# Kernel tuning notes

Hardware: AMD Instinct MI355X
Metric: run time of the kernel (lower is better)

The kernel has to match this reference:

```python
import jax, jax.numpy as jnp
import numpy as np

T, B, I, H, C, O = 4096, 8, 256, 512, 1024, 512
SCHEDULE = 1.0
UPPER_T = 0.3
NIND = int((1.0 - SCHEDULE) * (C - 2) * UPPER_T) + 1  # = 1 (argmax WTA)


def setup_inputs() -> dict:
    key = jax.random.key(0)
    ks = jax.random.split(key, 8)
    def lin(k, fan_out, fan_in):
        s = 1.0 / np.sqrt(fan_in)
        kw, kb = jax.random.split(k)
        return (jax.random.uniform(kw, (fan_out, fan_in), jnp.float32, -s, s),
                jax.random.uniform(kb, (fan_out,), jnp.float32, -s, s))
    i2m_w, i2m_b = lin(ks[0], H, I)
    m2h_w, m2h_b = lin(ks[1], C, H)
    h2o_w, h2o_b = lin(ks[2], O, C)
    return {
        "x": jax.random.normal(ks[3], (T, B, I), jnp.float32),
        "hidden1": jnp.zeros((1,), jnp.float32),  # unused dummy (overwritten in torch forward)
        "i2m_w": i2m_w, "i2m_b": i2m_b,
        "m2h_w": m2h_w, "m2h_b": m2h_b,
        "h2o_w": h2o_w, "h2o_b": h2o_b,
    }


def reference(x, hidden1, i2m_w, i2m_b, m2h_w, m2h_b, h2o_w, h2o_b):
    # linear -> relu
    h = jax.nn.relu(jnp.einsum('tbi,hi->tbh', x, i2m_w) + i2m_b)
    # linear -> relu -> concept pre-activations [T,B,C]
    c = jax.nn.relu(jnp.einsum('tbh,ch->tbc', h, m2h_w) + m2h_b)
    # winner-take-all: top-Nind scatter mask (replaces CPU argsort round-trip)
    _, idx = jax.lax.top_k(c, NIND)  # [T,B,NIND]
    t_ix = jnp.arange(c.shape[0])[:, None, None]
    b_ix = jnp.arange(c.shape[1])[None, :, None]
    mask = jnp.zeros_like(c).at[t_ix, b_ix, idx].set(1.0)
    m = c * mask
    # L2 normalize over concept axis
    m = m / jnp.linalg.norm(m, axis=-1, keepdims=True)
    out = jnp.einsum('tbc,oc->tbo', m, h2o_w) + h2o_b
    return jax.nn.log_softmax(out, axis=-1)
```

## Files before the change

### kernel.cpp

```cpp
#include <hip/hip_runtime.h>
#include <stdint.h>

#define M_ROWS 32768
#define I_DIM 256
#define H_DIM 512
#define C_DIM 1024
#define O_DIM 512

typedef __attribute__((ext_vector_type(8))) short bf16x8;
typedef __attribute__((ext_vector_type(4))) float f32x4;

__device__ __forceinline__ ushort bf16_rne(float f) {
    unsigned u = __float_as_uint(f);
    unsigned r = u + 0x7FFFu + ((u >> 16) & 1u);
    return (ushort)(r >> 16);
}
__device__ __forceinline__ float bf16_f32(ushort h) {
    return __uint_as_float(((unsigned)h) << 16);
}
__device__ __forceinline__ void split2(float f, ushort& hi, ushort& mid) {
    hi = bf16_rne(f);
    mid = bf16_rne(f - bf16_f32(hi));
}

__device__ __forceinline__ void async_ld16(const void* g, void* l) {
    __builtin_amdgcn_global_load_lds(
        (const __attribute__((address_space(1))) void*)g,
        (__attribute__((address_space(3))) void*)l, 16, 0, 0);
}

__device__ __forceinline__ unsigned long long packvi(float v, int col) {
    unsigned u = __float_as_uint(v);
    u = (u & 0x80000000u) ? ~u : (u | 0x80000000u);
    return ((unsigned long long)u << 32) | (unsigned)(~col);
}

__device__ __forceinline__ int slot_of(int kc, int row) {
    return (kc + ((row >> 1) & 3)) & 3;
}

__global__ __launch_bounds__(256)
void prep(const float* __restrict__ W1, ushort* __restrict__ w1h, ushort* __restrict__ w1m,
          const float* __restrict__ W2, ushort* __restrict__ w2h, ushort* __restrict__ w2m,
          const float* __restrict__ Wo, const float* __restrict__ bo,
          float* __restrict__ LS, unsigned long long* __restrict__ part) {
    __shared__ float sred[4];
    const int b = blockIdx.x;
    const int t = threadIdx.x;
    if (b < 320) {
        const int isW1 = (b < 64);
        const float* W = isW1 ? W1 : W2;
        ushort* hh = isW1 ? w1h : w2h;
        ushort* mm = isW1 ? w1m : w2m;
        const int K = isW1 ? I_DIM : H_DIM;
        const int cpr = K >> 3;
        int gid = (isW1 ? b : b - 64) * 256 + t;
        int row = gid / cpr;
        int rem = gid - row * cpr;
        int g = rem >> 2, kc = rem & 3;
        float4 v0 = *(const float4*)(W + (size_t)gid * 8);
        float4 v1 = *(const float4*)(W + (size_t)gid * 8 + 4);
        __align__(16) ushort h[8], m[8];
        float f[8];
        *(float4*)&f[0] = v0; *(float4*)&f[4] = v1;
        #pragma unroll
        for (int j = 0; j < 8; ++j) split2(f[j], h[j], m[j]);
        size_t dst = (size_t)row * K + g * 32 + slot_of(kc, row) * 8;
        *(uint4*)(hh + dst) = *(uint4*)h;
        *(uint4*)(mm + dst) = *(uint4*)m;
    } else if (b < 1344) {
        const int j = b - 320;
        float l0 = Wo[(size_t)t * C_DIM + j] + bo[t];
        float l1 = Wo[(size_t)(t + 256) * C_DIM + j] + bo[t + 256];

        float mx = fmaxf(l0, l1);
        #pragma unroll
        for (int off = 1; off < 64; off <<= 1)
            mx = fmaxf(mx, __shfl_xor(mx, off, 64));
        if ((t & 63) == 0) sred[t >> 6] = mx;
        __syncthreads();
        mx = fmaxf(fmaxf(sred[0], sred[1]), fmaxf(sred[2], sred[3]));
        __syncthreads();

        float s = expf(l0 - mx) + expf(l1 - mx);
        #pragma unroll
        for (int off = 1; off < 64; off <<= 1)
            s += __shfl_xor(s, off, 64);
        if ((t & 63) == 0) sred[t >> 6] = s;
        __syncthreads();
        s = sred[0] + sred[1] + sred[2] + sred[3];

        float lse = mx + logf(s);
        LS[(size_t)j * O_DIM + t] = l0 - lse;
        LS[(size_t)j * O_DIM + t + 256] = l1 - lse;
    } else {
        part[(b - 1344) * 256 + t] = 0ull;
    }
}

__global__ __launch_bounds__(256, 4)
void gemm1_mfma(const float* __restrict__ X, const ushort* __restrict__ W1h,
                const ushort* __restrict__ W1m, const float* __restrict__ b1,
                ushort* __restrict__ Hh, ushort* __restrict__ Hm) {
    __shared__ __align__(16) ushort LB[16384];
    ushort* As0 = LB;
    ushort* As1 = LB + 4096;
    ushort* Bs0 = LB + 8192;
    ushort* Bs1 = LB + 12288;

    const int tid = threadIdx.x;
    const int lane = tid & 63, wave = tid >> 6;
    const int wm = wave >> 1, wn = wave & 1;
    const int lcol = lane & 15, quad = lane >> 4;
    const int mBase = blockIdx.x * 128;
    const int nBase = blockIdx.y * 128;
    const int s_row = tid >> 1, s_half = tid & 1;
    const int bplane = wave >> 1;
    const ushort* wp = bplane ? W1m : W1h;
    const int brow0 = (wave & 1) * 64;
    const int lrow = lane >> 2, lk = (lane & 3) * 8;

    f32x4 acc[4][4];
    #pragma unroll
    for (int i = 0; i < 4; ++i)
        #pragma unroll
        for (int j = 0; j < 4; ++j)
            acc[i][j] = (f32x4){0.f, 0.f, 0.f, 0.f};

    int aoff[4], boff[4];
    #pragma unroll
    for (int t = 0; t < 4; ++t) {
        int ra = wm * 64 + t * 16 + lcol;
        int rb = wn * 64 + t * 16 + lcol;
        aoff[t] = ra * 32 + slot_of(quad, ra) * 8;
        boff[t] = rb * 32 + slot_of(quad, rb) * 8;
    }
    const int sl0 = slot_of(s_half * 2,     s_row);
    const int sl1 = slot_of(s_half * 2 + 1, s_row);

    for (int ks = 0; ks < I_DIM / 32; ++ks) {
        const int k0 = ks * 32;
        const float* ap = X + (size_t)(mBase + s_row) * I_DIM + k0 + s_half * 16;
        float4 f0 = ((const float4*)ap)[0];
        float4 f1 = ((const float4*)ap)[1];
        float4 f2 = ((const float4*)ap)[2];
        float4 f3 = ((const float4*)ap)[3];

        __syncthreads();

        #pragma unroll
        for (int i = 0; i < 4; ++i) {
            int r = brow0 + i * 16;
            const ushort* g = wp + (size_t)(nBase + r + lrow) * I_DIM + k0 + lk;
            async_ld16(g, (bplane ? Bs1 : Bs0) + r * 32);
        }

        float f[16];
        *(float4*)&f[0] = f0; *(float4*)&f[4] = f1;
        *(float4*)&f[8] = f2; *(float4*)&f[12] = f3;
        bf16x8 h0, h1, m0, m1;
        #pragma unroll
        for (int j = 0; j < 8; ++j) {
            ushort hu, mu;
            split2(f[j], hu, mu);
            h0[j] = (short)hu; m0[j] = (short)mu;
            split2(f[j + 8], hu, mu);
            h1[j] = (short)hu; m1[j] = (short)mu;
        }
        *(bf16x8*)&As0[s_row * 32 + sl0 * 8] = h0;
        *(bf16x8*)&As0[s_row * 32 + sl1 * 8] = h1;
        *(bf16x8*)&As1[s_row * 32 + sl0 * 8] = m0;
        *(bf16x8*)&As1[s_row * 32 + sl1 * 8] = m1;

        __syncthreads();

        bf16x8 af[4][2];
        #pragma unroll
        for (int mt = 0; mt < 4; ++mt) {
            af[mt][0] = *(const bf16x8*)&As0[aoff[mt]];
            af[mt][1] = *(const bf16x8*)&As1[aoff[mt]];
        }
        #pragma unroll
        for (int nt = 0; nt < 4; ++nt) {
            bf16x8 bh = *(const bf16x8*)&Bs0[boff[nt]];
            bf16x8 bm = *(const bf16x8*)&Bs1[boff[nt]];
            #pragma unroll
            for (int mt = 0; mt < 4; ++mt) {
                f32x4 a = acc[mt][nt];
                a = __builtin_amdgcn_mfma_f32_16x16x32_bf16(af[mt][1], bh, a, 0, 0, 0);
                a = __builtin_amdgcn_mfma_f32_16x16x32_bf16(af[mt][0], bm, a, 0, 0, 0);
                a = __builtin_amdgcn_mfma_f32_16x16x32_bf16(af[mt][0], bh, a, 0, 0, 0);
                acc[mt][nt] = a;
            }
        }
    }

    #pragma unroll
    for (int plane = 0; plane < 2; ++plane) {
        __syncthreads();
        #pragma unroll
        for (int nt = 0; nt < 4; ++nt) {
            int colRel = wn * 64 + nt * 16 + lcol;
            int g = colRel >> 5, kc = (colRel >> 3) & 3, pos = colRel & 7;
            float bias = b1[nBase + colRel];
            #pragma unroll
            for (int mt = 0; mt < 4; ++mt) {
                #pragma unroll
                for (int r = 0; r < 4; ++r) {
                    int rowRel = wm * 64 + mt * 16 + quad * 4 + r;
                    float v = fmaxf(acc[mt][nt][r] + bias, 0.f);
                    ushort hu, mu;
                    split2(v, hu, mu);
                    LB[rowRel * 128 + g * 32 + slot_of(kc, rowRel) * 8 + pos]
                        = plane ? mu : hu;
                }
            }
        }
        __syncthreads();
        ushort* dstp = plane ? Hm : Hh;
        #pragma unroll
        for (int l = 0; l < 8; ++l) {
            int c = l * 256 + tid;
            int row = c >> 4, idx = c & 15;
            *(uint4*)(dstp + (size_t)(mBase + row) * H_DIM + nBase + idx * 8)
                = *(const uint4*)&LB[row * 128 + idx * 8];
        }
    }
}

__global__ __launch_bounds__(512, 2)
void gemm2_mfma(const ushort* __restrict__ Hh, const ushort* __restrict__ Hm,
                const ushort* __restrict__ W2h, const ushort* __restrict__ W2m,
                const float* __restrict__ b2,
                unsigned long long* __restrict__ part) {
    __shared__ __align__(16) ushort As[2][2][8192];
    __shared__ __align__(16) ushort Bs[2][2][8192];
    const int tid = threadIdx.x;
    const int lane = tid & 63, wave = tid >> 6;
    const int wm = wave >> 2, wn = wave & 3;
    const int lcol = lane & 15, quad = lane >> 4;
    const int lrow = lane >> 2, lk = (lane & 3) * 8;

    const int d = blockIdx.x;
    const int l = d >> 3;
    const int mT = ((d & 7) << 4) + (l >> 2);
    const int nT = l & 3;
    const int mBase = mT * 256;
    const int nBase = nT * 256;

    const int m_id = wave >> 1;
    const int shalf = wave & 1;
    const ushort* gsrc;
    ushort* l0;
    ushort* l1;
    switch (m_id) {
        case 0:  gsrc = Hh  + (size_t)mBase * H_DIM; l0 = &As[0][0][0]; l1 = &As[1][0][0]; break;
        case 1:  gsrc = Hm  + (size_t)mBase * H_DIM; l0 = &As[0][1][0]; l1 = &As[1][1][0]; break;
        case 2:  gsrc = W2h + (size_t)nBase * H_DIM; l0 = &Bs[0][0][0]; l1 = &Bs[1][0][0]; break;
        default: gsrc = W2m + (size_t)nBase * H_DIM; l0 = &Bs[0][1][0]; l1 = &Bs[1][1][0]; break;
    }
    l0 += shalf * 4096;
    l1 += shalf * 4096;
    const ushort* gks = gsrc + (size_t)(shalf * 128 + lrow) * H_DIM + lk;

    f32x4 acc[8][4];
    #pragma unroll
    for (int i = 0; i < 8; ++i)
        #pragma unroll
        for (int j = 0; j < 4; ++j)
            acc[i][j] = (f32x4){0.f, 0.f, 0.f, 0.f};

    int aoff[8], boff[4];
    #pragma unroll
    for (int t = 0; t < 8; ++t) {
        int ra = wm * 128 + t * 16 + lcol;
        aoff[t] = ra * 32 + slot_of(quad, ra) * 8;
    }
    #pragma unroll
    for (int t = 0; t < 4; ++t) {
        int rb = wn * 64 + t * 16 + lcol;
        boff[t] = rb * 32 + slot_of(quad, rb) * 8;
    }

    auto stage = [&](ushort* lb, int k0) {
        #pragma unroll
        for (int j = 0; j < 8; ++j)
            async_ld16(gks + k0 + (size_t)(j * 16) * H_DIM, lb + j * 512);
    };

    stage(l0, 0);
    asm volatile("s_waitcnt vmcnt(0)" ::: "memory");
    __builtin_amdgcn_s_barrier();
    __builtin_amdgcn_sched_barrier(0);

    const int NK = H_DIM / 32;
    #pragma unroll 2
    for (int ks = 0; ks < NK; ++ks) {
        const int cur = ks & 1;
        if (ks < NK - 1) {
            stage(cur ? l0 : l1, (ks + 1) * 32);
            __builtin_amdgcn_sched_barrier(0);
        }

        bf16x8 bh[4], bm[4];
        #pragma unroll
        for (int nt = 0; nt < 4; ++nt) {
            bh[nt] = *(const bf16x8*)&Bs[cur][0][boff[nt]];
            bm[nt] = *(const bf16x8*)&Bs[cur][1][boff[nt]];
        }
        #pragma unroll
        for (int half = 0; half < 2; ++half) {
            bf16x8 ah[4], am[4];
            #pragma unroll
            for (int mt = 0; mt < 4; ++mt) {
                ah[mt] = *(const bf16x8*)&As[cur][0][aoff[half * 4 + mt]];
                am[mt] = *(const bf16x8*)&As[cur][1][aoff[half * 4 + mt]];
            }
            __builtin_amdgcn_s_setprio(1);
            #pragma unroll
            for (int nt = 0; nt < 4; ++nt) {
                #pragma unroll
                for (int mt = 0; mt < 4; ++mt) {
                    f32x4 a = acc[half * 4 + mt][nt];
                    a = __builtin_amdgcn_mfma_f32_16x16x32_bf16(am[mt], bh[nt], a, 0, 0, 0);
                    a = __builtin_amdgcn_mfma_f32_16x16x32_bf16(ah[mt], bm[nt], a, 0, 0, 0);
                    a = __builtin_amdgcn_mfma_f32_16x16x32_bf16(ah[mt], bh[nt], a, 0, 0, 0);
                    acc[half * 4 + mt][nt] = a;
                }
            }
            __builtin_amdgcn_s_setprio(0);
        }

        if (ks < NK - 1)
            asm volatile("s_waitcnt vmcnt(0)" ::: "memory");
        __builtin_amdgcn_s_barrier();
        __builtin_amdgcn_sched_barrier(0);
    }

    float bias[4];
    #pragma unroll
    for (int nt = 0; nt < 4; ++nt)
        bias[nt] = b2[nBase + wn * 64 + nt * 16 + lcol];

    #pragma unroll
    for (int mt = 0; mt < 8; ++mt) {
        #pragma unroll
        for (int r = 0; r < 4; ++r) {
            unsigned long long best = 0ull;
            #pragma unroll
            for (int nt = 0; nt < 4; ++nt) {
                int col = nBase + wn * 64 + nt * 16 + lcol;
                float v = acc[mt][nt][r] + bias[nt];
                unsigned long long p = packvi(v, col);
                if (p > best) best = p;
            }
            #pragma unroll
            for (int off = 1; off < 16; off <<= 1) {
                unsigned long long o = __shfl_xor((long long)best, off, 64);
                if (o > best) best = o;
            }
            if (lcol == 0) {
                int row = mBase + wm * 128 + mt * 16 + quad * 4 + r;
                atomicMax(&part[row], best);
            }
        }
    }
}

__global__ __launch_bounds__(256)
void gather_out(const unsigned long long* __restrict__ part,
                const float* __restrict__ LS, float* __restrict__ out) {
    const int tid = threadIdx.x;
    const int row = blockIdx.x * 2 + (tid >> 7);
    const int q = tid & 127;
    unsigned long long best = part[row];
    unsigned u = (unsigned)(best >> 32);
    float v = (u & 0x80000000u) ? __uint_as_float(u ^ 0x80000000u)
                                : __uint_as_float(~u);
    int col = (int)(~(unsigned)best) & (C_DIM - 1);
    int j = (v > 0.f) ? col : 0;
    float4 val = ((const float4*)LS)[(size_t)j * 128 + q];
    ((float4*)out)[(size_t)row * 128 + q] = val;
}

extern "C" void kernel_launch(void* const* d_in, const int* in_sizes, int n_in,
                              void* d_out, int out_size, void* d_ws, size_t ws_size,
                              hipStream_t stream) {
    const float* x     = (const float*)d_in[0];
    const float* i2m_w = (const float*)d_in[2];
    const float* i2m_b = (const float*)d_in[3];
    const float* m2h_w = (const float*)d_in[4];
    const float* m2h_b = (const float*)d_in[5];
    const float* h2o_w = (const float*)d_in[6];
    const float* h2o_b = (const float*)d_in[7];
    float* out = (float*)d_out;

    char* ws = (char*)d_ws;
    ushort* w1h = (ushort*)(ws);
    ushort* w1m = (ushort*)(ws + 262144);
    ushort* w2h = (ushort*)(ws + 524288);
    ushort* w2m = (ushort*)(ws + 1572864);
    float*  LS  = (float*)(ws + 2621440);
    unsigned long long* part = (unsigned long long*)(ws + 4718592);

    ushort* Hh = (ushort*)d_out;
    ushort* Hm = Hh + (size_t)M_ROWS * H_DIM;

    prep<<<1472, 256, 0, stream>>>(i2m_w, w1h, w1m, m2h_w, w2h, w2m,
                                   h2o_w, h2o_b, LS, part);
    gemm1_mfma<<<dim3(M_ROWS / 128, H_DIM / 128), 256, 0, stream>>>(
        x, w1h, w1m, i2m_b, Hh, Hm);
    gemm2_mfma<<<(M_ROWS / 256) * (C_DIM / 256), 512, 0, stream>>>(
        Hh, Hm, w2h, w2m, m2h_b, part);
    gather_out<<<M_ROWS / 2, 256, 0, stream>>>(part, LS, out);
}
```

Measured before the change: 244.5 us.

## Split GEMM k-step into four phases interleaving LDS reads, async loads and MFMAs

Restructures the inner k-loop of the concept GEMM into four sub-phases, each covering a quarter of the output tile. Each phase issues its own LDS fragment reads. The next tile's global-to-LDS async loads are split across the first two phases, with barriers placed so the waves stay in lockstep. The aim is to spread memory traffic evenly between MFMA bursts and to lower register pressure by holding fewer B fragments at once. In exchange it adds more barriers per k-step and reloads the A fragments twice.

```diff
diff --git a/kernel.cpp b/kernel.cpp
--- a/kernel.cpp
+++ b/kernel.cpp
@@ -282,13 +282,15 @@
         boff[t] = rb * 32 + slot_of(quad, rb) * 8;
     }
 
-    auto stage = [&](ushort* lb, int k0) {
-        #pragma unroll
-        for (int j = 0; j < 8; ++j)
-            async_ld16(gks + k0 + (size_t)(j * 16) * H_DIM, lb + j * 512);
+    auto stage4 = [&](ushort* lb, int k0, int jb) {
+        #pragma unroll
+        for (int j = 0; j < 4; ++j)
+            async_ld16(gks + k0 + (size_t)((jb + j) * 16) * H_DIM,
+                       lb + (jb + j) * 512);
     };
 
-    stage(l0, 0);
+    stage4(l0, 0, 0);
+    stage4(l0, 0, 4);
     asm volatile("s_waitcnt vmcnt(0)" ::: "memory");
     __builtin_amdgcn_s_barrier();
     __builtin_amdgcn_sched_barrier(0);
@@ -297,44 +299,56 @@
     #pragma unroll 2
     for (int ks = 0; ks < NK; ++ks) {
         const int cur = ks & 1;
-        if (ks < NK - 1) {
-            stage(cur ? l0 : l1, (ks + 1) * 32);
+        ushort* nxt = cur ? l0 : l1;
+        const bool more = (ks + 1 < NK);
+
+        #pragma unroll
+        for (int ph = 0; ph < 4; ++ph) {
+            const int mh = ph >> 1, nh = ph & 1;
+
+            bf16x8 ah[4], am[4], bh[2], bm[2];
+            #pragma unroll
+            for (int mt = 0; mt < 4; ++mt) {
+                ah[mt] = *(const bf16x8*)&As[cur][0][aoff[mh * 4 + mt]];
+                am[mt] = *(const bf16x8*)&As[cur][1][aoff[mh * 4 + mt]];
+            }
+            #pragma unroll
+            for (int nt = 0; nt < 2; ++nt) {
+                bh[nt] = *(const bf16x8*)&Bs[cur][0][boff[nh * 2 + nt]];
+                bm[nt] = *(const bf16x8*)&Bs[cur][1][boff[nh * 2 + nt]];
+            }
+
+            if (more && ph < 2) stage4(nxt, (ks + 1) * 32, ph * 4);
+
+            __builtin_amdgcn_s_barrier();
+            asm volatile("s_waitcnt lgkmcnt(0)" ::: "memory");
             __builtin_amdgcn_sched_barrier(0);
-        }
-
-        bf16x8 bh[4], bm[4];
-        #pragma unroll
-        for (int nt = 0; nt < 4; ++nt) {
-            bh[nt] = *(const bf16x8*)&Bs[cur][0][boff[nt]];
-            bm[nt] = *(const bf16x8*)&Bs[cur][1][boff[nt]];
-        }
-        #pragma unroll
-        for (int half = 0; half < 2; ++half) {
-            bf16x8 ah[4], am[4];
-            #pragma unroll
-            for (int mt = 0; mt < 4; ++mt) {
-                ah[mt] = *(const bf16x8*)&As[cur][0][aoff[half * 4 + mt]];
-                am[mt] = *(const bf16x8*)&As[cur][1][aoff[half * 4 + mt]];
-            }
+
             __builtin_amdgcn_s_setprio(1);
             #pragma unroll
-            for (int nt = 0; nt < 4; ++nt) {
+            for (int nt = 0; nt < 2; ++nt) {
                 #pragma unroll
                 for (int mt = 0; mt < 4; ++mt) {
-                    f32x4 a = acc[half * 4 + mt][nt];
+                    f32x4 a = acc[mh * 4 + mt][nh * 2 + nt];
                     a = __builtin_amdgcn_mfma_f32_16x16x32_bf16(am[mt], bh[nt], a, 0, 0, 0);
                     a = __builtin_amdgcn_mfma_f32_16x16x32_bf16(ah[mt], bm[nt], a, 0, 0, 0);
                     a = __builtin_amdgcn_mfma_f32_16x16x32_bf16(ah[mt], bh[nt], a, 0, 0, 0);
-                    acc[half * 4 + mt][nt] = a;
+                    acc[mh * 4 + mt][nh * 2 + nt] = a;
                 }
             }
             __builtin_amdgcn_s_setprio(0);
-        }
-
-        if (ks < NK - 1)
-            asm volatile("s_waitcnt vmcnt(0)" ::: "memory");
-        __builtin_amdgcn_s_barrier();
-        __builtin_amdgcn_sched_barrier(0);
+
+            if (ph == 3) {
+                if (more) {
+                    asm volatile("s_waitcnt vmcnt(0)" ::: "memory");
+                    __builtin_amdgcn_s_barrier();
+                    __builtin_amdgcn_sched_barrier(0);
+                }
+            } else {
+                __builtin_amdgcn_s_barrier();
+                __builtin_amdgcn_sched_barrier(0);
+            }
+        }
     }
 
     float bias[4];
```

After: 256.1 us. 4.7% more time.

## Enlarge gemm1 to 256x256 tiles with double-buffered LDS pipeline

Applied to the files above, without the earlier changes.

gemm1 moves from 128x128 tiles with 256 threads to 256x256 tiles with 512 threads, which raises operand reuse per block. The K loop now double-buffers the A and B tiles in LDS, prefetching the next slice of X and W while the MFMAs run, and uses a single barrier per step. It also remaps the block index so that neighbouring blocks share M-tiles, and raises wave priority around the MFMA section. In exchange it uses 128KB of LDS and more accumulator registers per thread, which limits occupancy to one or two blocks per CU.

```diff
diff --git a/kernel.cpp b/kernel.cpp
--- a/kernel.cpp
+++ b/kernel.cpp
@@ -98,66 +98,70 @@
     }
 }
 
-__global__ __launch_bounds__(256, 4)
+__global__ __launch_bounds__(512, 2)
 void gemm1_mfma(const float* __restrict__ X, const ushort* __restrict__ W1h,
                 const ushort* __restrict__ W1m, const float* __restrict__ b1,
                 ushort* __restrict__ Hh, ushort* __restrict__ Hm) {
-    __shared__ __align__(16) ushort LB[16384];
-    ushort* As0 = LB;
-    ushort* As1 = LB + 4096;
-    ushort* Bs0 = LB + 8192;
-    ushort* Bs1 = LB + 12288;
+    __shared__ __align__(16) ushort SMEM[65536];
 
     const int tid = threadIdx.x;
     const int lane = tid & 63, wave = tid >> 6;
-    const int wm = wave >> 1, wn = wave & 1;
+    const int wm = wave >> 2, wn = wave & 3;
     const int lcol = lane & 15, quad = lane >> 4;
-    const int mBase = blockIdx.x * 128;
-    const int nBase = blockIdx.y * 128;
+    const int lrow = lane >> 2, lk = (lane & 3) * 8;
+
+    const int d = blockIdx.x;
+    const int q = d >> 3;
+    const int mT = ((d & 7) << 4) + (q >> 1);
+    const int nT = q & 1;
+    const int mBase = mT * 256;
+    const int nBase = nT * 256;
+
     const int s_row = tid >> 1, s_half = tid & 1;
-    const int bplane = wave >> 1;
+    const int sl0 = slot_of(s_half * 2,     s_row);
+    const int sl1 = slot_of(s_half * 2 + 1, s_row);
+    const float* xrow = X + (size_t)(mBase + s_row) * I_DIM + s_half * 16;
+
+    const int bplane = wave >> 2;
+    const int brow0 = (wave & 3) * 64;
     const ushort* wp = bplane ? W1m : W1h;
-    const int brow0 = (wave & 1) * 64;
-    const int lrow = lane >> 2, lk = (lane & 3) * 8;
-
-    f32x4 acc[4][4];
-    #pragma unroll
-    for (int i = 0; i < 4; ++i)
+    const ushort* gks = wp + (size_t)(nBase + brow0 + lrow) * I_DIM + lk;
+
+    f32x4 acc[8][4];
+    #pragma unroll
+    for (int i = 0; i < 8; ++i)
         #pragma unroll
         for (int j = 0; j < 4; ++j)
             acc[i][j] = (f32x4){0.f, 0.f, 0.f, 0.f};
 
-    int aoff[4], boff[4];
+    int aoff[8], boff[4];
+    #pragma unroll
+    for (int t = 0; t < 8; ++t) {
+        int ra = wm * 128 + t * 16 + lcol;
+        aoff[t] = ra * 32 + slot_of(quad, ra) * 8;
+    }
     #pragma unroll
     for (int t = 0; t < 4; ++t) {
-        int ra = wm * 64 + t * 16 + lcol;
         int rb = wn * 64 + t * 16 + lcol;
-        aoff[t] = ra * 32 + slot_of(quad, ra) * 8;
         boff[t] = rb * 32 + slot_of(quad, rb) * 8;
     }
-    const int sl0 = slot_of(s_half * 2,     s_row);
-    const int sl1 = slot_of(s_half * 2 + 1, s_row);
-
-    for (int ks = 0; ks < I_DIM / 32; ++ks) {
-        const int k0 = ks * 32;
-        const float* ap = X + (size_t)(mBase + s_row) * I_DIM + k0 + s_half * 16;
-        float4 f0 = ((const float4*)ap)[0];
-        float4 f1 = ((const float4*)ap)[1];
-        float4 f2 = ((const float4*)ap)[2];
-        float4 f3 = ((const float4*)ap)[3];
-
-        __syncthreads();
-
-        #pragma unroll
-        for (int i = 0; i < 4; ++i) {
-            int r = brow0 + i * 16;
-            const ushort* g = wp + (size_t)(nBase + r + lrow) * I_DIM + k0 + lk;
-            async_ld16(g, (bplane ? Bs1 : Bs0) + r * 32);
-        }
-
-        float f[16];
-        *(float4*)&f[0] = f0; *(float4*)&f[4] = f1;
-        *(float4*)&f[8] = f2; *(float4*)&f[12] = f3;
+
+    auto loadX = [&](float* f, int k0) {
+        const float* ap = xrow + k0;
+        *(float4*)&f[0]  = ((const float4*)ap)[0];
+        *(float4*)&f[4]  = ((const float4*)ap)[1];
+        *(float4*)&f[8]  = ((const float4*)ap)[2];
+        *(float4*)&f[12] = ((const float4*)ap)[3];
+    };
+    auto stageB = [&](int buf, int k0) {
+        ushort* bb = SMEM + 32768 + buf * 16384 + bplane * 8192 + brow0 * 32;
+        #pragma unroll
+        for (int j = 0; j < 4; ++j)
+            async_ld16(gks + k0 + (size_t)(j * 16) * I_DIM, bb + j * 512);
+    };
+    auto writeA = [&](int buf, const float* f) {
+        ushort* a0 = SMEM + buf * 16384;
+        ushort* a1 = a0 + 8192;
         bf16x8 h0, h1, m0, m1;
         #pragma unroll
         for (int j = 0; j < 8; ++j) {
@@ -167,32 +171,75 @@
             split2(f[j + 8], hu, mu);
             h1[j] = (short)hu; m1[j] = (short)mu;
         }
-        *(bf16x8*)&As0[s_row * 32 + sl0 * 8] = h0;
-        *(bf16x8*)&As0[s_row * 32 + sl1 * 8] = h1;
-        *(bf16x8*)&As1[s_row * 32 + sl0 * 8] = m0;
-        *(bf16x8*)&As1[s_row * 32 + sl1 * 8] = m1;
-
-        __syncthreads();
-
-        bf16x8 af[4][2];
-        #pragma unroll
-        for (int mt = 0; mt < 4; ++mt) {
-            af[mt][0] = *(const bf16x8*)&As0[aoff[mt]];
-            af[mt][1] = *(const bf16x8*)&As1[aoff[mt]];
-        }
+        *(bf16x8*)&a0[s_row * 32 + sl0 * 8] = h0;
+        *(bf16x8*)&a0[s_row * 32 + sl1 * 8] = h1;
+        *(bf16x8*)&a1[s_row * 32 + sl0 * 8] = m0;
+        *(bf16x8*)&a1[s_row * 32 + sl1 * 8] = m1;
+    };
+
+    {
+        float fx[16];
+        loadX(fx, 0);
+        stageB(0, 0);
+        writeA(0, fx);
+    }
+    asm volatile("s_waitcnt lgkmcnt(0)" ::: "memory");
+    asm volatile("s_waitcnt vmcnt(0)" ::: "memory");
+    __builtin_amdgcn_s_barrier();
+    __builtin_amdgcn_sched_barrier(0);
+
+    const int NK = I_DIM / 32;
+    #pragma unroll 2
+    for (int ks = 0; ks < NK; ++ks) {
+        const int cur = ks & 1;
+        const bool more = (ks + 1 < NK);
+        const ushort* Ac0 = SMEM + cur * 16384;
+        const ushort* Ac1 = Ac0 + 8192;
+        const ushort* Bc0 = SMEM + 32768 + cur * 16384;
+        const ushort* Bc1 = Bc0 + 8192;
+
+        float fn[16];
+        if (more) {
+            loadX(fn, (ks + 1) * 32);
+            stageB(cur ^ 1, (ks + 1) * 32);
+            __builtin_amdgcn_sched_barrier(0);
+        }
+
+        bf16x8 bh[4], bm[4];
         #pragma unroll
         for (int nt = 0; nt < 4; ++nt) {
-            bf16x8 bh = *(const bf16x8*)&Bs0[boff[nt]];
-            bf16x8 bm = *(const bf16x8*)&Bs1[boff[nt]];
+            bh[nt] = *(const bf16x8*)&Bc0[boff[nt]];
+            bm[nt] = *(const bf16x8*)&Bc1[boff[nt]];
+        }
+        #pragma unroll
+        for (int half = 0; half < 2; ++half) {
+            bf16x8 ah[4], am[4];
             #pragma unroll
             for (int mt = 0; mt < 4; ++mt) {
-                f32x4 a = acc[mt][nt];
-                a = __builtin_amdgcn_mfma_f32_16x16x32_bf16(af[mt][1], bh, a, 0, 0, 0);
-                a = __builtin_amdgcn_mfma_f32_16x16x32_bf16(af[mt][0], bm, a, 0, 0, 0);
-                a = __builtin_amdgcn_mfma_f32_16x16x32_bf16(af[mt][0], bh, a, 0, 0, 0);
-                acc[mt][nt] = a;
-            }
-        }
+                ah[mt] = *(const bf16x8*)&Ac0[aoff[half * 4 + mt]];
+                am[mt] = *(const bf16x8*)&Ac1[aoff[half * 4 + mt]];
+            }
+            __builtin_amdgcn_s_setprio(1);
+            #pragma unroll
+            for (int nt = 0; nt < 4; ++nt) {
+                #pragma unroll
+                for (int mt = 0; mt < 4; ++mt) {
+                    f32x4 a = acc[half * 4 + mt][nt];
+                    a = __builtin_amdgcn_mfma_f32_16x16x32_bf16(am[mt], bh[nt], a, 0, 0, 0);
+                    a = __builtin_amdgcn_mfma_f32_16x16x32_bf16(ah[mt], bm[nt], a, 0, 0, 0);
+                    a = __builtin_amdgcn_mfma_f32_16x16x32_bf16(ah[mt], bh[nt], a, 0, 0, 0);
+                    acc[half * 4 + mt][nt] = a;
+                }
+            }
+            __builtin_amdgcn_s_setprio(0);
+        }
+
+        if (more) writeA(cur ^ 1, fn);
+        asm volatile("s_waitcnt lgkmcnt(0)" ::: "memory");
+        if (more)
+            asm volatile("s_waitcnt vmcnt(0)" ::: "memory");
+        __builtin_amdgcn_s_barrier();
+        __builtin_amdgcn_sched_barrier(0);
     }
 
     #pragma unroll
@@ -204,14 +251,14 @@
             int g = colRel >> 5, kc = (colRel >> 3) & 3, pos = colRel & 7;
             float bias = b1[nBase + colRel];
             #pragma unroll
-            for (int mt = 0; mt < 4; ++mt) {
+            for (int mt = 0; mt < 8; ++mt) {
                 #pragma unroll
                 for (int r = 0; r < 4; ++r) {
-                    int rowRel = wm * 64 + mt * 16 + quad * 4 + r;
+                    int rowRel = wm * 128 + mt * 16 + quad * 4 + r;
                     float v = fmaxf(acc[mt][nt][r] + bias, 0.f);
                     ushort hu, mu;
                     split2(v, hu, mu);
-                    LB[rowRel * 128 + g * 32 + slot_of(kc, rowRel) * 8 + pos]
+                    SMEM[rowRel * 256 + g * 32 + slot_of(kc, rowRel) * 8 + pos]
                         = plane ? mu : hu;
                 }
             }
@@ -219,11 +266,11 @@
         __syncthreads();
         ushort* dstp = plane ? Hm : Hh;
         #pragma unroll
-        for (int l = 0; l < 8; ++l) {
-            int c = l * 256 + tid;
-            int row = c >> 4, idx = c & 15;
+        for (int l2 = 0; l2 < 16; ++l2) {
+            int c = l2 * 512 + tid;
+            int row = c >> 5, idx = c & 31;
             *(uint4*)(dstp + (size_t)(mBase + row) * H_DIM + nBase + idx * 8)
-                = *(const uint4*)&LB[row * 128 + idx * 8];
+                = *(const uint4*)&SMEM[row * 256 + idx * 8];
         }
     }
 }
@@ -408,7 +455,7 @@
 
     prep<<<1472, 256, 0, stream>>>(i2m_w, w1h, w1m, m2h_w, w2h, w2m,
                                    h2o_w, h2o_b, LS, part);
-    gemm1_mfma<<<dim3(M_ROWS / 128, H_DIM / 128), 256, 0, stream>>>(
+    gemm1_mfma<<<(M_ROWS / 256) * (H_DIM / 256), 512, 0, stream>>>(
         x, w1h, w1m, i2m_b, Hh, Hm);
     gemm2_mfma<<<(M_ROWS / 256) * (C_DIM / 256), 512, 0, stream>>>(
         Hh, Hm, w2h, w2m, m2h_b, part);
```

Result: no change. 242.0 us (-1.0%).
